# Performance work log

Hardware: AMD Instinct MI355X
Metric: run time of the kernel (lower is better)

The kernel has to match this reference:

```python
import jax, jax.numpy as jnp
import numpy as np

LN_EPS = 1e-5

def _layer_norm(x, gamma, beta):
    mu = jnp.mean(x, axis=-1, keepdims=True)
    var = jnp.mean(jnp.square(x - mu), axis=-1, keepdims=True)
    return (x - mu) * jax.lax.rsqrt(var + LN_EPS) * gamma + beta

def setup_inputs() -> dict:
    key = jax.random.key(0)
    ks = jax.random.split(key, 10)
    B, S, D_IN = 8, 2048, 1024
    H1, H2, C = 2048, 1024, 64
    s1 = 1.0 / np.sqrt(D_IN)
    s2 = 1.0 / np.sqrt(H1)
    s3 = 1.0 / np.sqrt(H2)
    return {
        "embeddings": jax.random.normal(ks[0], (B, S, D_IN), jnp.float32),
        "prior_evidence": jax.random.normal(ks[1], (B, C), jnp.float32),
        "W1": jax.random.uniform(ks[2], (D_IN, H1), jnp.float32, -s1, s1),
        "b1": jnp.zeros((H1,), jnp.float32),
        "g1": jnp.ones((H1,), jnp.float32),
        "beta1": jnp.zeros((H1,), jnp.float32),
        "W2": jax.random.uniform(ks[3], (H1, H2), jnp.float32, -s2, s2),
        "b2": jnp.zeros((H2,), jnp.float32),
        "g2": jnp.ones((H2,), jnp.float32),
        "beta2": jnp.zeros((H2,), jnp.float32),
        "Wh": jax.random.uniform(ks[4], (H2, C), jnp.float32, -s3, s3),
        "bh": jnp.zeros((C,), jnp.float32),
        "and_gate": jnp.ones((C,), jnp.float32),
        "or_gate": jnp.ones((C,), jnp.float32),
    }

def reference(embeddings, prior_evidence, W1, b1, g1, beta1, W2, b2, g2, beta2, Wh, bh, and_gate, or_gate):
    # feature extractor: Linear -> ReLU -> Dropout(eval: identity) -> LayerNorm, x2
    h = _layer_norm(jax.nn.relu(embeddings @ W1 + b1), g1, beta1)
    features = _layer_norm(jax.nn.relu(h @ W2 + b2), g2, beta2)  # [B,S,H2]
    d = features.shape[-1]
    scores = jnp.einsum('bsd,btd->bst', features, features) / jnp.sqrt(jnp.float32(d))
    attention_weights = jax.nn.softmax(scores, axis=-1)          # [B,S,S]
    attended = jnp.einsum('bst,btd->bsd', attention_weights, features)
    logits = attended @ Wh + bh                                   # [B,S,C]
    sig_l = jax.nn.sigmoid(logits)
    sig_p = jax.nn.sigmoid(prior_evidence)[:, None, :]            # [B,1,C] broadcasts
    and_ev = jnp.minimum(sig_l, sig_p) * and_gate
    or_ev = jnp.maximum(sig_l, sig_p) * or_gate
    logits = jnp.log((and_ev + or_ev) / 2 + 1e-10)
    return (logits, attention_weights)
```

## Files before the change

kernel.cpp:

```cpp
#include <hip/hip_runtime.h>

typedef unsigned short u16;
typedef __bf16 bf16x8 __attribute__((ext_vector_type(8)));
typedef float f32x4 __attribute__((ext_vector_type(4)));

__device__ __forceinline__ u16 f2bf(float f) {
    unsigned u = __float_as_uint(f);
    u = (u + 0x7FFFu + ((u >> 16) & 1u)) >> 16;
    return (u16)u;
}
__device__ __forceinline__ float bf2f(u16 h) {
    return __uint_as_float(((unsigned)h) << 16);
}

__device__ __forceinline__ void gld16(const u16* g, u16* l) {
    __builtin_amdgcn_global_load_lds((const __attribute__((address_space(1))) void*)g,
                                     (__attribute__((address_space(3))) void*)l, 16, 0, 0);
}

__device__ __forceinline__ int swz(int row, int col) {
    return ((row >> 4) * 2 + (col >> 5)) * 512 + (row & 15) * 32 +
           ((col & 31) ^ ((row & 8) ? 16 : 0));
}

__global__ __launch_bounds__(256) void cvt_kernel(const float* __restrict__ in,
                                                  u16* __restrict__ out, long n) {
    long i = ((long)blockIdx.x * blockDim.x + threadIdx.x) * 4;
    if (i + 3 < n) {
        float4 v = *(const float4*)&in[i];
        __align__(8) u16 r[4] = {f2bf(v.x), f2bf(v.y), f2bf(v.z), f2bf(v.w)};
        *(int2*)&out[i] = *(const int2*)r;
    }
}

template <int INF32>
__global__ __launch_bounds__(256) void transpose_to_bf16(const void* __restrict__ in,
                                                         u16* __restrict__ out, int R, int C,
                                                         long inB, long outB) {
    __shared__ float tile[32][33];
    const long zi = (long)blockIdx.z * inB;
    const long zo = (long)blockIdx.z * outB;
    const int c0 = blockIdx.x * 32, r0 = blockIdx.y * 32;
    const int tx = threadIdx.x & 31;
    const int ty = threadIdx.x >> 5;
#pragma unroll
    for (int i = 0; i < 32; i += 8) {
        long idx = zi + (long)(r0 + ty + i) * C + c0 + tx;
        float v = INF32 ? ((const float*)in)[idx] : bf2f(((const u16*)in)[idx]);
        tile[ty + i][tx] = v;
    }
    __syncthreads();
#pragma unroll
    for (int i = 0; i < 32; i += 8) {
        out[zo + (long)(c0 + ty + i) * R + r0 + tx] = f2bf(tile[tx][ty + i]);
    }
}

template <int OUTBF>
__global__ __launch_bounds__(512, 2) void gemm_nt(const u16* __restrict__ A,
                                                  const u16* __restrict__ Bm,
                                                  void* __restrict__ Cout, int M, int N, int K,
                                                  long sA, long sB, long sC,
                                                  const float* __restrict__ bias, int act,
                                                  float scale, int symm,
                                                  const float* __restrict__ rscale) {
    int bx, by, zz;
    if (symm) {
        const int q = gridDim.x >> 3;
        const int orig = blockIdx.x;
        const int wgid = (orig & 7) * q + (orig >> 3);
        const int NB = N >> 8;
        const int nTri = (NB * (NB + 1)) >> 1;
        zz = wgid / nTri;
        int t = wgid - zz * nTri;
        by = 0;
        int rem = NB;
        while (t >= rem) {
            t -= rem;
            --rem;
            ++by;
        }
        bx = by + t;
    } else {
        const int nx = gridDim.x;
        const int nwg = nx * gridDim.y;
        const int orig = blockIdx.y * nx + blockIdx.x;
        const int q = nwg >> 3, r = nwg & 7, xcd = orig & 7, o8 = orig >> 3;
        const int wgid = (xcd < r ? xcd * (q + 1) : r * (q + 1) + (xcd - r) * q) + o8;
        if (r == 0 && (q % nx) == 0) {
            const int rpc = q / nx;
            const int o = wgid - xcd * q;
            by = xcd * rpc + (o % rpc);
            bx = o / rpc;
        } else {
            bx = wgid % nx;
            by = wgid / nx;
        }
        zz = blockIdx.z;
    }

    __shared__ __align__(16) u16 SM[67584];
    u16(*As)[256 * 64] = (u16(*)[256 * 64])SM;
    u16(*Bs)[256 * 64] = (u16(*)[256 * 64])(SM + 32768);
    u16* T = SM;
    const int tid = threadIdx.x;
    const int lane = tid & 63;
    const int wid = tid >> 6;
    const int wr = wid >> 2;
    const int wc = wid & 3;
    const int l15 = lane & 15, lg = lane >> 4;
    const long zA = (long)zz * sA;
    const long zB = (long)zz * sB;
    const long zC = (long)zz * sC;
    const int m0 = by * 256, n0 = bx * 256;
    const u16* Ab = A + zA + (long)m0 * K;
    const u16* Bb = Bm + zB + (long)n0 * K;
    const int nt = K >> 6;

    f32x4 acc[8][4] = {};

    auto stage_chunk = [&](int t, int b, int j) {
        const int c = j * 512 + tid;
        const int s = c >> 6, r = (c >> 2) & 15;
        const int row = (s >> 1) * 16 + r;
        const int col = (s & 1) * 32 + (((c & 3) * 8) ^ ((r & 8) ? 16 : 0));
        gld16(Ab + (long)row * K + t * 64 + col, &As[b][c * 8]);
        gld16(Bb + (long)row * K + t * 64 + col, &Bs[b][c * 8]);
    };

#pragma unroll
    for (int j = 0; j < 4; ++j) stage_chunk(0, 0, j);
    asm volatile("s_waitcnt vmcnt(0)" ::: "memory");
    __builtin_amdgcn_s_barrier();

    for (int t = 0; t < nt; ++t) {
        const int cur = t & 1;
        if (t + 1 < nt) {
#pragma unroll
            for (int j = 0; j < 4; ++j) stage_chunk(t + 1, cur ^ 1, j);
        }
        bf16x8 bf[4][2];
#pragma unroll
        for (int n = 0; n < 4; ++n)
#pragma unroll
            for (int kk = 0; kk < 2; ++kk)
                bf[n][kk] = *(const bf16x8*)&Bs[cur][swz(wc * 64 + n * 16 + l15, kk * 32 + lg * 8)];
        bf16x8 af[2][2][2];
#pragma unroll
        for (int mi = 0; mi < 2; ++mi)
#pragma unroll
            for (int kk = 0; kk < 2; ++kk)
                af[0][mi][kk] =
                    *(const bf16x8*)&As[cur][swz(wr * 128 + mi * 16 + l15, kk * 32 + lg * 8)];
#pragma unroll
        for (int mg = 0; mg < 4; ++mg) {
            if (mg < 3) {
#pragma unroll
                for (int mi = 0; mi < 2; ++mi)
#pragma unroll
                    for (int kk = 0; kk < 2; ++kk)
                        af[(mg + 1) & 1][mi][kk] = *(const bf16x8*)&As[cur][swz(
                            wr * 128 + (mg + 1) * 32 + mi * 16 + l15, kk * 32 + lg * 8)];
            }
            __builtin_amdgcn_s_setprio(1);
#pragma unroll
            for (int mi = 0; mi < 2; ++mi)
#pragma unroll
                for (int n = 0; n < 4; ++n)
#pragma unroll
                    for (int kk = 0; kk < 2; ++kk)
                        acc[mg * 2 + mi][n] = __builtin_amdgcn_mfma_f32_16x16x32_bf16(
                            af[mg & 1][mi][kk], bf[n][kk], acc[mg * 2 + mi][n], 0, 0, 0);
            __builtin_amdgcn_s_setprio(0);
        }
        __builtin_amdgcn_s_barrier();
        asm volatile("s_waitcnt vmcnt(0)" ::: "memory");
        __builtin_amdgcn_s_barrier();
    }

    const int mirror = symm && (bx > by);
#pragma unroll
    for (int n = 0; n < 4; ++n) {
        const int col = n0 + wc * 64 + n * 16 + l15;
        const float bv = bias ? bias[col] : 0.0f;
#pragma unroll
        for (int m = 0; m < 8; ++m) {
            const int rowb = m0 + wr * 128 + m * 16 + lg * 4;
            float v[4];
#pragma unroll
            for (int r = 0; r < 4; ++r) {
                float f = acc[m][n][r] * scale + bv;
                if (act == 1)
                    f = fmaxf(f, 0.0f);
                else if (act == 2)
                    f = __expf(f - 32.0f);
                if (rscale) f *= rscale[(long)zz * M + rowb + r];
                v[r] = f;
                if (OUTBF)
                    ((u16*)Cout)[zC + (long)(rowb + r) * N + col] = f2bf(f);
                else
                    ((float*)Cout)[zC + (long)(rowb + r) * N + col] = f;
            }
            if (mirror) {
                if (OUTBF) {
                    const int cl = wc * 64 + n * 16 + l15;
                    const int rl = wr * 128 + m * 16 + lg * 4;
                    __align__(8) u16 tv[4] = {f2bf(v[0]), f2bf(v[1]), f2bf(v[2]), f2bf(v[3])};
                    *(int2*)&T[cl * 264 + rl] = *(const int2*)tv;
                } else {
                    *(float4*)&((float*)Cout)[zC + (long)col * N + rowb] =
                        make_float4(v[0], v[1], v[2], v[3]);
                }
            }
        }
    }
    if (mirror && OUTBF) {
        __builtin_amdgcn_s_barrier();
#pragma unroll
        for (int i = 0; i < 16; ++i) {
            const int c = i * 512 + tid;
            const int tr = c >> 5, tc = c & 31;
            *(int4*)&((u16*)Cout)[zC + (long)(n0 + tr) * N + m0 + tc * 8] =
                *(const int4*)&T[tr * 264 + tc * 8];
        }
    }
}

template <int CH>
__global__ __launch_bounds__(256) void ln_wave(u16* __restrict__ x, const float* __restrict__ g,
                                               const float* __restrict__ be) {
    const int lane = threadIdx.x & 63;
    const int wid = threadIdx.x >> 6;
    const long row = (long)blockIdx.x * 4 + wid;
    u16* p = x + row * (CH * 512);
    __align__(16) u16 raw[CH][8];
    float s = 0.f, ss = 0.f;
#pragma unroll
    for (int c = 0; c < CH; ++c) {
        *(int4*)raw[c] = *(const int4*)&p[(c * 64 + lane) * 8];
#pragma unroll
        for (int j = 0; j < 8; ++j) {
            float f = bf2f(raw[c][j]);
            s += f;
            ss += f * f;
        }
    }
#pragma unroll
    for (int o = 1; o < 64; o <<= 1) {
        s += __shfl_xor(s, o);
        ss += __shfl_xor(ss, o);
    }
    const float inv = 1.0f / (float)(CH * 512);
    const float mu = s * inv;
    const float var = ss * inv - mu * mu;
    const float rs = rsqrtf(var + 1e-5f);
#pragma unroll
    for (int c = 0; c < CH; ++c) {
        const int base = (c * 64 + lane) * 8;
        float4 g0 = *(const float4*)&g[base];
        float4 g1 = *(const float4*)&g[base + 4];
        float4 b0 = *(const float4*)&be[base];
        float4 b1 = *(const float4*)&be[base + 4];
        float gv[8] = {g0.x, g0.y, g0.z, g0.w, g1.x, g1.y, g1.z, g1.w};
        float bv[8] = {b0.x, b0.y, b0.z, b0.w, b1.x, b1.y, b1.z, b1.w};
#pragma unroll
        for (int j = 0; j < 8; ++j)
            raw[c][j] = f2bf((bf2f(raw[c][j]) - mu) * rs * gv[j] + bv[j]);
        *(int4*)&p[base] = *(const int4*)raw[c];
    }
}

__global__ __launch_bounds__(256) void norm_wave(const u16* __restrict__ e,
                                                 float* __restrict__ outw,
                                                 float* __restrict__ rowInv) {
    const int lane = threadIdx.x & 63;
    const int wid = threadIdx.x >> 6;
    const long row = (long)blockIdx.x * 4 + wid;
    const u16* p = e + row * 2048;
    float v[4][8];
    float s = 0.f;
#pragma unroll
    for (int c = 0; c < 4; ++c) {
        __align__(16) u16 raw[8];
        *(int4*)raw = *(const int4*)&p[(c * 64 + lane) * 8];
#pragma unroll
        for (int j = 0; j < 8; ++j) {
            v[c][j] = bf2f(raw[j]);
            s += v[c][j];
        }
    }
#pragma unroll
    for (int o = 1; o < 64; o <<= 1) s += __shfl_xor(s, o);
    const float inv = 1.0f / s;
    if (lane == 0) rowInv[row] = inv;
    float* q = outw + row * 2048;
#pragma unroll
    for (int c = 0; c < 4; ++c) {
        const int base = (c * 64 + lane) * 8;
        float4 o0 = make_float4(v[c][0] * inv, v[c][1] * inv, v[c][2] * inv, v[c][3] * inv);
        float4 o1 = make_float4(v[c][4] * inv, v[c][5] * inv, v[c][6] * inv, v[c][7] * inv);
        *(float4*)&q[base] = o0;
        *(float4*)&q[base + 4] = o1;
    }
}

__global__ __launch_bounds__(256) void head_kernel(const u16* __restrict__ A,
                                                   const u16* __restrict__ WhT,
                                                   const float* __restrict__ bh,
                                                   const float* __restrict__ prior,
                                                   const float* __restrict__ ag,
                                                   const float* __restrict__ og,
                                                   float* __restrict__ out) {
    __shared__ __align__(16) u16 As2[128 * 64];
    __shared__ __align__(16) u16 Bs2[64 * 64];
    const int tid = threadIdx.x;
    const int lane = tid & 63;
    const int wid = tid >> 6;
    const int l15 = lane & 15, lg = lane >> 4;
    const int m0 = blockIdx.x * 128;
    const int srow = tid >> 3, scol = (tid & 7) * 8;
    const u16* pa = A + (long)(m0 + srow) * 1024 + scol;
    const u16* pb = WhT + (long)srow * 1024 + scol;

    f32x4 acc[2][4] = {};
    for (int k0 = 0; k0 < 1024; k0 += 64) {
#pragma unroll
        for (int i = 0; i < 4; ++i) gld16(pa + (long)i * 32 * 1024 + k0, &As2[i * 2048 + tid * 8]);
#pragma unroll
        for (int i = 0; i < 2; ++i) gld16(pb + (long)i * 32 * 1024 + k0, &Bs2[i * 2048 + tid * 8]);
        __syncthreads();
#pragma unroll
        for (int kk = 0; kk < 2; ++kk) {
            bf16x8 af[2], bfr[4];
#pragma unroll
            for (int m = 0; m < 2; ++m)
                af[m] = *(const bf16x8*)&As2[(wid * 32 + m * 16 + l15) * 64 + kk * 32 + lg * 8];
#pragma unroll
            for (int n = 0; n < 4; ++n)
                bfr[n] = *(const bf16x8*)&Bs2[(n * 16 + l15) * 64 + kk * 32 + lg * 8];
#pragma unroll
            for (int m = 0; m < 2; ++m)
#pragma unroll
                for (int n = 0; n < 4; ++n)
                    acc[m][n] =
                        __builtin_amdgcn_mfma_f32_16x16x32_bf16(af[m], bfr[n], acc[m][n], 0, 0, 0);
        }
        __syncthreads();
    }

#pragma unroll
    for (int n = 0; n < 4; ++n) {
        const int col = n * 16 + l15;
        const float bhv = bh[col];
        const float agv = ag[col];
        const float ogv = og[col];
#pragma unroll
        for (int m = 0; m < 2; ++m) {
#pragma unroll
            for (int r = 0; r < 4; ++r) {
                const int row = m0 + wid * 32 + m * 16 + lg * 4 + r;
                const float logit = acc[m][n][r] + bhv;
                const int b = row >> 11;
                const float sp = 1.f / (1.f + expf(-prior[b * 64 + col]));
                const float sl = 1.f / (1.f + expf(-logit));
                const float av = fminf(sl, sp) * agv;
                const float ov = fmaxf(sl, sp) * ogv;
                out[(long)row * 64 + col] = logf((av + ov) * 0.5f + 1e-10f);
            }
        }
    }
}

extern "C" void kernel_launch(void* const* d_in, const int* in_sizes, int n_in, void* d_out,
                              int out_size, void* d_ws, size_t ws_size, hipStream_t stream) {
    const float* emb = (const float*)d_in[0];
    const float* prior = (const float*)d_in[1];
    const float* W1 = (const float*)d_in[2];
    const float* b1 = (const float*)d_in[3];
    const float* g1 = (const float*)d_in[4];
    const float* be1 = (const float*)d_in[5];
    const float* W2 = (const float*)d_in[6];
    const float* b2 = (const float*)d_in[7];
    const float* g2 = (const float*)d_in[8];
    const float* be2 = (const float*)d_in[9];
    const float* Wh = (const float*)d_in[10];
    const float* bh = (const float*)d_in[11];
    const float* ag = (const float*)d_in[12];
    const float* og = (const float*)d_in[13];

    const int Bn = 8, S = 2048, DIN = 1024, H1 = 2048, H2 = 1024, Cc = 64;
    const int M = Bn * S;

    char* ws = (char*)d_ws;
    size_t off = 0;
    auto alloc = [&](size_t b) {
        size_t o = off;
        off += (b + 255) & ~(size_t)255;
        return o;
    };
    char* R0 = ws + alloc((size_t)M * H1 * 2);
    char* R1 = ws + alloc((size_t)M * DIN * 2);
    char* R2 = ws + alloc((size_t)M * H2 * 2);
    u16* W1t = (u16*)(ws + alloc((size_t)H1 * DIN * 2));
    u16* W2t = (u16*)(ws + alloc((size_t)H2 * H1 * 2));
    u16* WhT = (u16*)(ws + alloc((size_t)Cc * H2 * 2));
    float* rowInv = (float*)(ws + alloc((size_t)M * 4));

    u16* h = (u16*)R0;
    u16* attnb = (u16*)R0;
    u16* embb = (u16*)R1;
    u16* featT = (u16*)R1;
    u16* feat = (u16*)R2;
    u16* attd = (u16*)R2;

    float* out_logits = (float*)d_out;
    float* out_attn = out_logits + (size_t)M * Cc;

    cvt_kernel<<<(int)(((long)M * DIN) / 1024), 256, 0, stream>>>(emb, embb, (long)M * DIN);
    transpose_to_bf16<1><<<dim3(H1 / 32, DIN / 32, 1), 256, 0, stream>>>(W1, W1t, DIN, H1, 0, 0);
    transpose_to_bf16<1><<<dim3(H2 / 32, H1 / 32, 1), 256, 0, stream>>>(W2, W2t, H1, H2, 0, 0);
    transpose_to_bf16<1><<<dim3(Cc / 32, H2 / 32, 1), 256, 0, stream>>>(Wh, WhT, H2, Cc, 0, 0);
    gemm_nt<1><<<dim3(H1 / 256, M / 256, 1), 512, 0, stream>>>(embb, W1t, h, M, H1, DIN, 0, 0, 0,
                                                               b1, 1, 1.0f, 0, nullptr);
    ln_wave<4><<<M / 4, 256, 0, stream>>>(h, g1, be1);
    gemm_nt<1><<<dim3(H2 / 256, M / 256, 1), 512, 0, stream>>>(h, W2t, feat, M, H2, H1, 0, 0, 0,
                                                               b2, 1, 1.0f, 0, nullptr);
    ln_wave<2><<<M / 4, 256, 0, stream>>>(feat, g2, be2);
    transpose_to_bf16<0><<<dim3(H2 / 32, S / 32, Bn), 256, 0, stream>>>(
        feat, featT, S, H2, (long)S * H2, (long)H2 * S);
    {
        const int NB = S / 256;
        const int nTri = NB * (NB + 1) / 2;
        gemm_nt<1><<<dim3(nTri * Bn, 1, 1), 512, 0, stream>>>(
            feat, feat, attnb, S, S, H2, (long)S * H2, (long)S * H2, (long)S * S, nullptr,
            2, 0.03125f, 1, nullptr);
    }
    norm_wave<<<M / 4, 256, 0, stream>>>(attnb, out_attn, rowInv);
    gemm_nt<1><<<dim3(H2 / 256, S / 256, Bn), 512, 0, stream>>>(attnb, featT, attd, S, H2, S,
                                                                (long)S * S, (long)H2 * S,
                                                                (long)S * H2, nullptr, 0, 1.0f, 0,
                                                                rowInv);
    head_kernel<<<M / 128, 256, 0, stream>>>(attd, WhT, bh, prior, ag, og, out_logits);
}
```

Before: 458.1 us.

## Split GEMM K-tile into half stages with finer-grained load/compute interleaving

Restructures the main bf16 MFMA GEMM loop to stage each 64-wide K tile as two 32-wide halves per operand, using a new row-major XOR swizzle layout in LDS. Global-to-LDS loads for the next tile are issued in four quarter-stages interleaved between four MFMA phases, with partial vmcnt waits and extra barriers. The aim is to overlap async copies with MFMA work more evenly and cut LDS bank conflicts. In exchange it adds more barriers per iteration and more fragile wait-count reasoning.

```diff
diff --git a/kernel.cpp b/kernel.cpp
--- a/kernel.cpp
+++ b/kernel.cpp
@@ -16,11 +16,6 @@
 __device__ __forceinline__ void gld16(const u16* g, u16* l) {
     __builtin_amdgcn_global_load_lds((const __attribute__((address_space(1))) void*)g,
                                      (__attribute__((address_space(3))) void*)l, 16, 0, 0);
-}
-
-__device__ __forceinline__ int swz(int row, int col) {
-    return ((row >> 4) * 2 + (col >> 5)) * 512 + (row & 15) * 32 +
-           ((col & 31) ^ ((row & 8) ? 16 : 0));
 }
 
 __global__ __launch_bounds__(256) void cvt_kernel(const float* __restrict__ in,
@@ -100,8 +95,6 @@
     }
 
     __shared__ __align__(16) u16 SM[67584];
-    u16(*As)[256 * 64] = (u16(*)[256 * 64])SM;
-    u16(*Bs)[256 * 64] = (u16(*)[256 * 64])(SM + 32768);
     u16* T = SM;
     const int tid = threadIdx.x;
     const int lane = tid & 63;
@@ -119,62 +112,106 @@
 
     f32x4 acc[8][4] = {};
 
-    auto stage_chunk = [&](int t, int b, int j) {
-        const int c = j * 512 + tid;
-        const int s = c >> 6, r = (c >> 2) & 15;
-        const int row = (s >> 1) * 16 + r;
-        const int col = (s & 1) * 32 + (((c & 3) * 8) ^ ((r & 8) ? 16 : 0));
-        gld16(Ab + (long)row * K + t * 64 + col, &As[b][c * 8]);
-        gld16(Bb + (long)row * K + t * 64 + col, &Bs[b][c * 8]);
+    auto stage_half = [&](int x, int half, int op) {
+#pragma unroll
+        for (int j = 0; j < 2; ++j) {
+            const int c = j * 512 + tid;
+            const int row = c >> 2;
+            const int col = (((c & 3) ^ ((row >> 1) & 3)) << 3);
+            const u16* src = (op ? Bb : Ab) + (long)row * K + x * 64 + half * 32 + col;
+            gld16(src, &SM[(op ? 32768 : 0) + (x & 1) * 16384 + half * 8192 + c * 8]);
+        }
     };
 
-#pragma unroll
-    for (int j = 0; j < 4; ++j) stage_chunk(0, 0, j);
-    asm volatile("s_waitcnt vmcnt(0)" ::: "memory");
+    stage_half(0, 0, 0);
+    stage_half(0, 0, 1);
+    stage_half(0, 1, 0);
+    stage_half(0, 1, 1);
+    asm volatile("s_waitcnt vmcnt(4)" ::: "memory");
     __builtin_amdgcn_s_barrier();
+
+    const int go = ((lg ^ ((l15 >> 1) & 3)) << 3);
 
     for (int t = 0; t < nt; ++t) {
         const int cur = t & 1;
+        const int aBase = cur * 16384, bBase = 32768 + cur * 16384;
+        bf16x8 bf[4], af[4];
+#pragma unroll
+        for (int n = 0; n < 4; ++n)
+            bf[n] = *(const bf16x8*)&SM[bBase + (wc * 64 + n * 16 + l15) * 32 + go];
+#pragma unroll
+        for (int m = 0; m < 4; ++m)
+            af[m] = *(const bf16x8*)&SM[aBase + (wr * 128 + m * 16 + l15) * 32 + go];
+        if (t + 1 < nt) stage_half(t + 1, 0, 0);
+        __builtin_amdgcn_s_barrier();
+        asm volatile("s_waitcnt lgkmcnt(0)" ::: "memory");
+        __builtin_amdgcn_sched_barrier(0);
+        __builtin_amdgcn_s_setprio(1);
+#pragma unroll
+        for (int m = 0; m < 4; ++m)
+#pragma unroll
+            for (int n = 0; n < 4; ++n)
+                acc[m][n] =
+                    __builtin_amdgcn_mfma_f32_16x16x32_bf16(af[m], bf[n], acc[m][n], 0, 0, 0);
+        __builtin_amdgcn_s_setprio(0);
+#pragma unroll
+        for (int m = 0; m < 4; ++m)
+            af[m] = *(const bf16x8*)&SM[aBase + (wr * 128 + 64 + m * 16 + l15) * 32 + go];
         if (t + 1 < nt) {
-#pragma unroll
-            for (int j = 0; j < 4; ++j) stage_chunk(t + 1, cur ^ 1, j);
-        }
-        bf16x8 bf[4][2];
+            stage_half(t + 1, 0, 1);
+            asm volatile("s_waitcnt vmcnt(4)" ::: "memory");
+        } else {
+            asm volatile("s_waitcnt vmcnt(0)" ::: "memory");
+        }
+        __builtin_amdgcn_s_barrier();
+        asm volatile("s_waitcnt lgkmcnt(0)" ::: "memory");
+        __builtin_amdgcn_sched_barrier(0);
+        __builtin_amdgcn_s_setprio(1);
+#pragma unroll
+        for (int m = 0; m < 4; ++m)
+#pragma unroll
+            for (int n = 0; n < 4; ++n)
+                acc[4 + m][n] = __builtin_amdgcn_mfma_f32_16x16x32_bf16(af[m], bf[n],
+                                                                        acc[4 + m][n], 0, 0, 0);
+        __builtin_amdgcn_s_setprio(0);
 #pragma unroll
         for (int n = 0; n < 4; ++n)
-#pragma unroll
-            for (int kk = 0; kk < 2; ++kk)
-                bf[n][kk] = *(const bf16x8*)&Bs[cur][swz(wc * 64 + n * 16 + l15, kk * 32 + lg * 8)];
-        bf16x8 af[2][2][2];
-#pragma unroll
-        for (int mi = 0; mi < 2; ++mi)
-#pragma unroll
-            for (int kk = 0; kk < 2; ++kk)
-                af[0][mi][kk] =
-                    *(const bf16x8*)&As[cur][swz(wr * 128 + mi * 16 + l15, kk * 32 + lg * 8)];
-#pragma unroll
-        for (int mg = 0; mg < 4; ++mg) {
-            if (mg < 3) {
-#pragma unroll
-                for (int mi = 0; mi < 2; ++mi)
-#pragma unroll
-                    for (int kk = 0; kk < 2; ++kk)
-                        af[(mg + 1) & 1][mi][kk] = *(const bf16x8*)&As[cur][swz(
-                            wr * 128 + (mg + 1) * 32 + mi * 16 + l15, kk * 32 + lg * 8)];
-            }
-            __builtin_amdgcn_s_setprio(1);
-#pragma unroll
-            for (int mi = 0; mi < 2; ++mi)
-#pragma unroll
-                for (int n = 0; n < 4; ++n)
-#pragma unroll
-                    for (int kk = 0; kk < 2; ++kk)
-                        acc[mg * 2 + mi][n] = __builtin_amdgcn_mfma_f32_16x16x32_bf16(
-                            af[mg & 1][mi][kk], bf[n][kk], acc[mg * 2 + mi][n], 0, 0, 0);
-            __builtin_amdgcn_s_setprio(0);
-        }
-        __builtin_amdgcn_s_barrier();
-        asm volatile("s_waitcnt vmcnt(0)" ::: "memory");
+            bf[n] = *(const bf16x8*)&SM[bBase + 8192 + (wc * 64 + n * 16 + l15) * 32 + go];
+#pragma unroll
+        for (int m = 0; m < 4; ++m)
+            af[m] = *(const bf16x8*)&SM[aBase + 8192 + (wr * 128 + m * 16 + l15) * 32 + go];
+        if (t + 1 < nt) stage_half(t + 1, 1, 0);
+        __builtin_amdgcn_s_barrier();
+        asm volatile("s_waitcnt lgkmcnt(0)" ::: "memory");
+        __builtin_amdgcn_sched_barrier(0);
+        __builtin_amdgcn_s_setprio(1);
+#pragma unroll
+        for (int m = 0; m < 4; ++m)
+#pragma unroll
+            for (int n = 0; n < 4; ++n)
+                acc[m][n] =
+                    __builtin_amdgcn_mfma_f32_16x16x32_bf16(af[m], bf[n], acc[m][n], 0, 0, 0);
+        __builtin_amdgcn_s_setprio(0);
+#pragma unroll
+        for (int m = 0; m < 4; ++m)
+            af[m] = *(const bf16x8*)&SM[aBase + 8192 + (wr * 128 + 64 + m * 16 + l15) * 32 + go];
+        if (t + 1 < nt) {
+            stage_half(t + 1, 1, 1);
+            asm volatile("s_waitcnt vmcnt(4)" ::: "memory");
+        } else {
+            asm volatile("s_waitcnt vmcnt(0)" ::: "memory");
+        }
+        __builtin_amdgcn_s_barrier();
+        asm volatile("s_waitcnt lgkmcnt(0)" ::: "memory");
+        __builtin_amdgcn_sched_barrier(0);
+        __builtin_amdgcn_s_setprio(1);
+#pragma unroll
+        for (int m = 0; m < 4; ++m)
+#pragma unroll
+            for (int n = 0; n < 4; ++n)
+                acc[4 + m][n] = __builtin_amdgcn_mfma_f32_16x16x32_bf16(af[m], bf[n],
+                                                                        acc[4 + m][n], 0, 0, 0);
+        __builtin_amdgcn_s_setprio(0);
         __builtin_amdgcn_s_barrier();
     }
 
```

After: 472.7 us. +3.2%, slower.
